# Kernel optimization log

Measured on AMD Instinct MI355X. Metric: run time of the kernel, lower is better.

Reference implementation:

```python
import jax, jax.numpy as jnp
import numpy as np

FEAT_STRIDE = 16
NMS_THRESH = 0.7
PRE_NMS = 6000   # eval mode: n_test_pre_nms
POST_NMS = 300   # eval mode: n_test_post_nms
MIN_SIZE = 16
NEG = jnp.float32(-1e30)


def _base_anchors(base_size=16, ratios=(0.5, 1.0, 2.0), scales=(8, 16, 32)):
    ctr = (base_size - 1) / 2.0
    size = float(base_size * base_size)
    out = []
    for r in ratios:
        w = np.round(np.sqrt(size / r))
        h = np.round(w * r)
        for s in scales:
            ws, hs = w * s, h * s
            out.append([ctr - 0.5 * (ws - 1), ctr - 0.5 * (hs - 1),
                        ctr + 0.5 * (ws - 1), ctr + 0.5 * (hs - 1)])
    return np.asarray(out, dtype=np.float32)  # (9,4)


def _all_anchors(feat_h, feat_w):
    base = _base_anchors()
    sx = np.arange(feat_w, dtype=np.float32) * FEAT_STRIDE
    sy = np.arange(feat_h, dtype=np.float32) * FEAT_STRIDE
    gx, gy = np.meshgrid(sx, sy)                      # (H,W)
    shifts = np.stack([gx, gy, gx, gy], axis=-1).reshape(-1, 1, 4)
    anchors = (shifts + base[None, :, :]).reshape(-1, 4)  # (H*W*9,4), order (h,w,a)
    return jnp.asarray(anchors)


def _nms_keep(boxes):
    # boxes sorted by descending score; torchvision IoU convention (no +1)
    n = boxes.shape[0]
    area = (boxes[:, 2] - boxes[:, 0]) * (boxes[:, 3] - boxes[:, 1])
    lt = jnp.maximum(boxes[:, None, :2], boxes[None, :, :2])  # (N,N,2)
    rb = jnp.minimum(boxes[:, None, 2:], boxes[None, :, 2:])
    wh = jnp.clip(rb - lt, 0.0)
    inter = wh[..., 0] * wh[..., 1]
    iou = inter / (area[:, None] + area[None, :] - inter)
    over = iou > NMS_THRESH
    idx = jnp.arange(n)

    def body(i, supp):
        row = over[i] & (idx > i) & jnp.logical_not(supp[i])
        return supp | row

    supp = jax.lax.fori_loop(0, n, body, jnp.zeros((n,), bool))
    keep = jnp.nonzero(~supp, size=POST_NMS, fill_value=0)[0]
    return keep


def reference(rpn_cls_scores, rpn_bbox_preds, img_h, img_w):
    feat_h, feat_w = rpn_cls_scores.shape[2], rpn_cls_scores.shape[3]
    anchors = _all_anchors(feat_h, feat_w)                      # (K,4)
    scores = jax.nn.softmax(
        rpn_cls_scores.transpose(0, 2, 3, 1).reshape(-1, 2), axis=1)[:, 1]
    deltas = rpn_bbox_preds.transpose(0, 2, 3, 1).reshape(-1, 4)

    widths = anchors[:, 2] - anchors[:, 0] + 1.0
    heights = anchors[:, 3] - anchors[:, 1] + 1.0
    ctr_x = anchors[:, 0] + 0.5 * widths
    ctr_y = anchors[:, 1] + 0.5 * heights
    dx, dy, dw, dh = deltas[:, 0], deltas[:, 1], deltas[:, 2], deltas[:, 3]
    pcx = dx * widths + ctr_x
    pcy = dy * heights + ctr_y
    pw = jnp.exp(dw) * widths
    ph = jnp.exp(dh) * heights

    x1 = jnp.clip(pcx - 0.5 * pw, 0.0, img_w - 1)
    y1 = jnp.clip(pcy - 0.5 * ph, 0.0, img_h - 1)
    x2 = jnp.clip(pcx + 0.5 * pw, 0.0, img_w - 1)
    y2 = jnp.clip(pcy + 0.5 * ph, 0.0, img_h - 1)
    proposals = jnp.stack([x1, y1, x2, y2], axis=1)             # (K,4)

    valid = ((x2 - x1 + 1.0) >= MIN_SIZE) & ((y2 - y1 + 1.0) >= MIN_SIZE)
    masked = jnp.where(valid, scores, NEG)
    _, order = jax.lax.top_k(masked, PRE_NMS)                   # sort desc + pre-nms cut
    boxes = proposals[order]                                    # (PRE_NMS,4)

    keep = _nms_keep(boxes)
    kept = boxes[keep]                                          # (POST_NMS,4)
    batch_inds = jnp.zeros((POST_NMS, 1), dtype=kept.dtype)
    return jnp.concatenate([batch_inds, kept], axis=1)          # (POST_NMS,5)


def setup_inputs() -> dict:
    key = jax.random.key(0)
    k1, k2 = jax.random.split(key)
    rpn_cls_scores = jax.random.normal(k1, (1, 18, 64, 100), dtype=jnp.float32)
    rpn_bbox_preds = 0.2 * jax.random.normal(k2, (1, 36, 64, 100), dtype=jnp.float32)
    return {"rpn_cls_scores": rpn_cls_scores, "rpn_bbox_preds": rpn_bbox_preds,
            "img_h": 1024, "img_w": 1600}
```

## Files before the change

### kernel.cpp

```cpp
#include <hip/hip_runtime.h>

typedef unsigned long long u64;
typedef unsigned int u32;

#define FEAT_W 100
#define NANCH 9
#define NTOT 57600
#define NPAD 65536
#define PRE_NMS 6000
#define POST_NMS 300
#define NBLK 94
#define NCHUNK 24
#define CH_STRIDE 6400
#define CHUNK 1024
#define CAP 6144

__constant__ double c_base[9][4] = {
    {-84.0, -40.0, 99.0, 55.0},    {-176.0, -88.0, 191.0, 103.0},
    {-360.0, -184.0, 375.0, 199.0},{-56.0, -56.0, 71.0, 71.0},
    {-120.0, -120.0, 135.0, 135.0},{-248.0, -248.0, 263.0, 263.0},
    {-36.0, -80.0, 51.0, 95.0},    {-80.0, -168.0, 95.0, 183.0},
    {-168.0, -344.0, 183.0, 359.0}};

struct BoxD { double x1, y1, x2, y2; };

__device__ __forceinline__ int packed_off(int i) {
  int q = i >> 6, r = i & 63;
  return 94 * i - 32 * q * (q - 1) - r * q;
}

__device__ __forceinline__ BoxD decode_box(int i, const float* __restrict__ bbox,
                                           double imw1, double imh1) {
  int pos = i / NANCH;
  int a = i - pos * NANCH;
  int h = pos / FEAT_W;
  int w = pos - h * FEAT_W;
  double ax1 = c_base[a][0] + 16.0 * (double)w;
  double ay1 = c_base[a][1] + 16.0 * (double)h;
  double ax2 = c_base[a][2] + 16.0 * (double)w;
  double ay2 = c_base[a][3] + 16.0 * (double)h;
  double wd = ax2 - ax1 + 1.0;
  double hg = ay2 - ay1 + 1.0;
  double cx = ax1 + 0.5 * wd;
  double cy = ay1 + 0.5 * hg;
  const float* bp = bbox + (size_t)(4 * a) * CH_STRIDE + pos;
  double dx = (double)bp[0];
  double dy = (double)bp[CH_STRIDE];
  double dw = (double)bp[2 * CH_STRIDE];
  double dh = (double)bp[3 * CH_STRIDE];
  double pcx = dx * wd + cx;
  double pcy = dy * hg + cy;
  double pw = exp(dw) * wd;
  double ph = exp(dh) * hg;
  BoxD b;
  b.x1 = fmin(fmax(pcx - 0.5 * pw, 0.0), imw1);
  b.y1 = fmin(fmax(pcy - 0.5 * ph, 0.0), imh1);
  b.x2 = fmin(fmax(pcx + 0.5 * pw, 0.0), imw1);
  b.y2 = fmin(fmax(pcy + 0.5 * ph, 0.0), imh1);
  return b;
}

__device__ __forceinline__ u64 score_key(int i, const float* __restrict__ cls,
                                         const float* __restrict__ bbox,
                                         double imw1, double imh1) {
  BoxD b = decode_box(i, bbox, imw1, imh1);
  bool valid = (b.x2 - b.x1 + 1.0 >= 16.0) && (b.y2 - b.y1 + 1.0 >= 16.0);
  int pos = i / NANCH;
  int a = i - pos * NANCH;
  double c0 = (double)cls[(size_t)(2 * a) * CH_STRIDE + pos];
  double c1 = (double)cls[(size_t)(2 * a + 1) * CH_STRIDE + pos];
  double m = fmax(c0, c1);
  double e0 = exp(c0 - m), e1 = exp(c1 - m);
  double s = e1 / (e0 + e1);
  double masked = valid ? s : (double)(-1e30f);
  u64 u = (u64)__double_as_longlong(masked);
  return (u >> 63) ? ~u : (u | 0x8000000000000000ULL);
}

__device__ __forceinline__ bool before(u64 ka, u32 va, u64 kb, u32 vb) {
  return (ka > kb) || (ka == kb && va < vb);
}
__device__ __forceinline__ bool comes_after(u64 ka, u32 va, u64 kb, u32 vb) {
  return (ka < kb) || (ka == kb && va > vb);
}

__global__ __launch_bounds__(512) void k_score_sort(
    const float* __restrict__ cls, const float* __restrict__ bbox,
    const int* __restrict__ imh, const int* __restrict__ imw,
    u64* __restrict__ keys, u32* __restrict__ vals) {
  __shared__ u64 sk[CHUNK];
  __shared__ u32 sv[CHUNK];
  int base = blockIdx.x * CHUNK;
  double imh1 = (double)(imh[0] - 1);
  double imw1 = (double)(imw[0] - 1);
  for (int t = threadIdx.x; t < CHUNK; t += 512) {
    int i = base + t;
    if (i < NTOT) { sk[t] = score_key(i, cls, bbox, imw1, imh1); sv[t] = (u32)i; }
    else { sk[t] = 0ULL; sv[t] = (u32)i; }
  }
  __syncthreads();
  bool prev_cross = false;
  for (int k = 2; k <= CHUNK; k <<= 1) {
    for (int j = k >> 1; j > 0; j >>= 1) {
      bool cross = (j >= 128);
      if (cross || prev_cross) __syncthreads();
      int t = threadIdx.x;
      int i = ((t & ~(j - 1)) << 1) | (t & (j - 1));
      int l = i | j;
      bool up = ((i & k) == 0);
      u64 ka = sk[i], kb = sk[l];
      u32 va = sv[i], vb = sv[l];
      if (comes_after(ka, va, kb, vb) == up) { sk[i] = kb; sv[i] = vb; sk[l] = ka; sv[l] = va; }
      prev_cross = cross;
    }
  }
  __syncthreads();
  for (int t = threadIdx.x; t < CHUNK; t += 512) { keys[base + t] = sk[t]; vals[base + t] = sv[t]; }
}


__global__ void k_merge1(const u64* __restrict__ Ak, const u32* __restrict__ Av,
                         u64* __restrict__ Bk, u32* __restrict__ Bv) {
  int gtid = blockIdx.x * blockDim.x + threadIdx.x;
  if (gtid >= NPAD) return;
  int lst = gtid >> 10, pos = gtid & 1023, grp = lst >> 2;
  u64 k = Ak[gtid]; u32 v = Av[gtid];
  int b0 = grp << 2;
  int q = lst & 3;
  int i0 = 0 + (0 >= q), i1 = 1 + (1 >= q), i2 = 2 + (2 >= q);
  const u64* K0 = Ak + (size_t)(b0 + i0) * 1024;
  const u64* K1 = Ak + (size_t)(b0 + i1) * 1024;
  const u64* K2 = Ak + (size_t)(b0 + i2) * 1024;
  const u32* V0 = Av + (size_t)(b0 + i0) * 1024;
  const u32* V1 = Av + (size_t)(b0 + i1) * 1024;
  const u32* V2 = Av + (size_t)(b0 + i2) * 1024;
  int lo0 = 0, hi0 = 1024, lo1 = 0, hi1 = 1024, lo2 = 0, hi2 = 1024;
  #pragma unroll
  for (int st = 0; st < 11; ++st) {
    int m0 = (lo0 + hi0) >> 1, m1 = (lo1 + hi1) >> 1, m2 = (lo2 + hi2) >> 1;
    int c0 = min(m0, 1023), c1 = min(m1, 1023), c2 = min(m2, 1023);
    u64 k0 = K0[c0], k1 = K1[c1], k2 = K2[c2];
    u32 v0 = V0[c0], v1 = V1[c1], v2 = V2[c2];
    if (lo0 < hi0) { if (before(k0, v0, k, v)) lo0 = m0 + 1; else hi0 = m0; }
    if (lo1 < hi1) { if (before(k1, v1, k, v)) lo1 = m1 + 1; else hi1 = m1; }
    if (lo2 < hi2) { if (before(k2, v2, k, v)) lo2 = m2 + 1; else hi2 = m2; }
  }
  int rank = pos + lo0 + lo1 + lo2;
  Bk[(size_t)grp * 4096 + rank] = k;
  Bv[(size_t)grp * 4096 + rank] = v;
}

__global__ void k_merge2(const u64* __restrict__ Bk, const u32* __restrict__ Bv,
                         u64* __restrict__ Ak, u32* __restrict__ Av) {
  int gtid = blockIdx.x * blockDim.x + threadIdx.x;
  if (gtid >= NPAD) return;
  int lst = gtid >> 12, pos = gtid & 4095, grp = lst >> 2;
  u64 k = Bk[gtid]; u32 v = Bv[gtid];
  int b0 = grp << 2;
  int q = lst & 3;
  int i0 = 0 + (0 >= q), i1 = 1 + (1 >= q), i2 = 2 + (2 >= q);
  const u64* K0 = Bk + (size_t)(b0 + i0) * 4096;
  const u64* K1 = Bk + (size_t)(b0 + i1) * 4096;
  const u64* K2 = Bk + (size_t)(b0 + i2) * 4096;
  const u32* V0 = Bv + (size_t)(b0 + i0) * 4096;
  const u32* V1 = Bv + (size_t)(b0 + i1) * 4096;
  const u32* V2 = Bv + (size_t)(b0 + i2) * 4096;
  int lo0 = 0, hi0 = 4096, lo1 = 0, hi1 = 4096, lo2 = 0, hi2 = 4096;
  #pragma unroll
  for (int st = 0; st < 13; ++st) {
    int m0 = (lo0 + hi0) >> 1, m1 = (lo1 + hi1) >> 1, m2 = (lo2 + hi2) >> 1;
    int c0 = min(m0, 4095), c1 = min(m1, 4095), c2 = min(m2, 4095);
    u64 k0 = K0[c0], k1 = K1[c1], k2 = K2[c2];
    u32 v0 = V0[c0], v1 = V1[c1], v2 = V2[c2];
    if (lo0 < hi0) { if (before(k0, v0, k, v)) lo0 = m0 + 1; else hi0 = m0; }
    if (lo1 < hi1) { if (before(k1, v1, k, v)) lo1 = m1 + 1; else hi1 = m1; }
    if (lo2 < hi2) { if (before(k2, v2, k, v)) lo2 = m2 + 1; else hi2 = m2; }
  }
  int rank = pos + lo0 + lo1 + lo2;
  if (rank < CAP) { Ak[(size_t)grp * CAP + rank] = k; Av[(size_t)grp * CAP + rank] = v; }
}

__global__ void k_merge3(const u64* __restrict__ Ak, const u32* __restrict__ Av,
                         const float* __restrict__ bbox, const int* __restrict__ imh,
                         const int* __restrict__ imw, double4* __restrict__ sboxes) {
  int gtid = blockIdx.x * blockDim.x + threadIdx.x;
  if (gtid >= 4 * CAP) return;
  int lst = gtid / CAP, pos = gtid - lst * CAP;
  u64 k = Ak[gtid]; u32 v = Av[gtid];
  int i0 = 0 + (0 >= lst), i1 = 1 + (1 >= lst), i2 = 2 + (2 >= lst);
  const u64* K0 = Ak + (size_t)i0 * CAP;
  const u64* K1 = Ak + (size_t)i1 * CAP;
  const u64* K2 = Ak + (size_t)i2 * CAP;
  const u32* V0 = Av + (size_t)i0 * CAP;
  const u32* V1 = Av + (size_t)i1 * CAP;
  const u32* V2 = Av + (size_t)i2 * CAP;
  int lo0 = 0, hi0 = CAP, lo1 = 0, hi1 = CAP, lo2 = 0, hi2 = CAP;
  #pragma unroll
  for (int st = 0; st < 13; ++st) {
    int m0 = (lo0 + hi0) >> 1, m1 = (lo1 + hi1) >> 1, m2 = (lo2 + hi2) >> 1;
    int c0 = min(m0, CAP - 1), c1 = min(m1, CAP - 1), c2 = min(m2, CAP - 1);
    u64 k0 = K0[c0], k1 = K1[c1], k2 = K2[c2];
    u32 v0 = V0[c0], v1 = V1[c1], v2 = V2[c2];
    if (lo0 < hi0) { if (before(k0, v0, k, v)) lo0 = m0 + 1; else hi0 = m0; }
    if (lo1 < hi1) { if (before(k1, v1, k, v)) lo1 = m1 + 1; else hi1 = m1; }
    if (lo2 < hi2) { if (before(k2, v2, k, v)) lo2 = m2 + 1; else hi2 = m2; }
  }
  int rank = pos + lo0 + lo1 + lo2;
  if (rank < PRE_NMS) {
    double imh1 = (double)(imh[0] - 1);
    double imw1 = (double)(imw[0] - 1);
    BoxD b = decode_box((int)v, bbox, imw1, imh1);
    sboxes[rank] = make_double4(b.x1, b.y1, b.x2, b.y2);
  }
}

__global__ void k_mask(const double4* __restrict__ sboxes, u64* __restrict__ mask,
                       u64* __restrict__ colC) {
  __shared__ double4 cb[64];
  int bc = blockIdx.x, br = blockIdx.y;
  int t = threadIdx.x;
  bool samechunk = (bc >> 2) == (br >> 2);
  if (bc < br) {
    if (samechunk) colC[(size_t)(((bc << 6) + t) * 4 + (br & 3))] = 0;
    return;
  }
  int j0 = bc * 64;
  int jt = j0 + t;
  cb[t] = (jt < PRE_NMS) ? sboxes[jt] : make_double4(0.0, 0.0, 0.0, 0.0);
  __syncthreads();
  int i = br * 64 + t;
  u64 bits = 0;
  if (i < PRE_NMS) {
    double4 rb = sboxes[i];
    double areai = (rb.z - rb.x) * (rb.w - rb.y);
    int cmax = min(64, PRE_NMS - j0);
    for (int c = 0; c < cmax; ++c) {
      int j = j0 + c;
      if (j <= i) continue;
      double4 cbx = cb[c];
      double xx1 = fmax(rb.x, cbx.x), yy1 = fmax(rb.y, cbx.y);
      double xx2 = fmin(rb.z, cbx.z), yy2 = fmin(rb.w, cbx.w);
      double w = fmax(xx2 - xx1, 0.0), h = fmax(yy2 - yy1, 0.0);
      double inter = w * h;
      double areaj = (cbx.z - cbx.x) * (cbx.w - cbx.y);
      if (inter > 0.7 * (areai + areaj - inter)) bits |= (1ULL << c);
    }
    mask[(size_t)(packed_off(i) + (bc - br))] = bits;
  }
  if (samechunk) {
    u64 colbits = 0;
    for (int j2 = 0; j2 < 64; ++j2) {
      u64 bl = __ballot(((bits >> j2) & 1ULL) != 0);
      if (t == j2) colbits = bl;
    }
    colC[(size_t)(((bc << 6) + t) * 4 + (br & 3))] = colbits;
  }
}

__device__ __forceinline__ u64 valid_word(int w) {
  int base = w << 6;
  if (base >= PRE_NMS) return 0ULL;
  if (base + 64 <= PRE_NMS) return ~0ULL;
  return (1ULL << (PRE_NMS - base)) - 1ULL;
}

__global__ __launch_bounds__(64) void k_scan(const u64* __restrict__ mask,
                                             const u64* __restrict__ colC,
                                             const double4* __restrict__ sboxes,
                                             float* __restrict__ out) {
  __shared__ int keepIdx[384];
  __shared__ int keepA[384];
  int lane = threadIdx.x;
  for (int r = lane; r < 384; r += 64) { keepIdx[r] = 0; keepA[r] = 0; }
  int nkeep = 0;
  bool done = false;

  u64 ct00, ct01, ct02, ct03, ct10, ct11, ct12, ct13;
  u64 ct20, ct21, ct22, ct23, ct30, ct31, ct32, ct33;

#define COL_LOAD(cc, T, a0, a1, a2, a3)                                        \
  {                                                                            \
    int J_ = ((cc) << 8) + ((T) << 6) + lane;                                  \
    a0 = 0; a1 = 0; a2 = 0; a3 = 0;                                            \
    if (J_ < PRE_NMS) {                                                        \
      const ulonglong2* p_ = (const ulonglong2*)(colC + (size_t)J_ * 4);       \
      ulonglong2 x_ = p_[0], y_ = p_[1];                                       \
      a0 = x_.x; a1 = x_.y; a2 = y_.x; a3 = y_.y;                              \
    }                                                                          \
  }

  COL_LOAD(0, 0, ct00, ct01, ct02, ct03)
  COL_LOAD(0, 1, ct10, ct11, ct12, ct13)
  COL_LOAD(0, 2, ct20, ct21, ct22, ct23)
  COL_LOAD(0, 3, ct30, ct31, ct32, ct33)

  for (int c = 0; c < NCHUNK && !done; ++c) {
    int wbase = c << 2;
    bool tail_ok = (wbase + 2) < NBLK;

    u64 n00 = 0, n01 = 0, n02 = 0, n03 = 0, n10 = 0, n11 = 0, n12 = 0, n13 = 0;
    u64 n20 = 0, n21 = 0, n22 = 0, n23 = 0, n30 = 0, n31 = 0, n32 = 0, n33 = 0;
    if (c + 1 < NCHUNK) {
      COL_LOAD(c + 1, 0, n00, n01, n02, n03)
      COL_LOAD(c + 1, 1, n10, n11, n12, n13)
      COL_LOAD(c + 1, 2, n20, n21, n22, n23)
      COL_LOAD(c + 1, 3, n30, n31, n32, n33)
    }

    int nq = (nkeep + 63) >> 6;
    int a0 = keepA[lane], a1 = keepA[64 + lane], a2 = keepA[128 + lane];
    int a3 = keepA[192 + lane], a4 = keepA[256 + lane];
    u64 g00 = 0, g01 = 0, g02 = 0, g03 = 0;
    u64 g10 = 0, g11 = 0, g12 = 0, g13 = 0;
    u64 g20 = 0, g21 = 0, g22 = 0, g23 = 0;
    u64 g30 = 0, g31 = 0, g32 = 0, g33 = 0;
    u64 g40 = 0, g41 = 0, g42 = 0, g43 = 0;
#define GATHER(AA, x0, x1, x2, x3)                                             \
    {                                                                          \
      const u64* p_ = mask + (size_t)(AA) + wbase;                             \
      x0 = p_[0];                                                              \
      x1 = p_[1];                                                              \
      if (tail_ok) { x2 = p_[2]; x3 = p_[3]; }                                 \
    }
    if (nq > 0) GATHER(a0, g00, g01, g02, g03)
    if (nq > 1) GATHER(a1, g10, g11, g12, g13)
    if (nq > 2) GATHER(a2, g20, g21, g22, g23)
    if (nq > 3) GATHER(a3, g30, g31, g32, g33)
    if (nq > 4) GATHER(a4, g40, g41, g42, g43)
#undef GATHER
    u64 or0 = 0, or1 = 0, or2 = 0, or3 = 0;
    if (lane < nkeep)       { or0 |= g00; or1 |= g01; or2 |= g02; or3 |= g03; }
    if (64 + lane < nkeep)  { or0 |= g10; or1 |= g11; or2 |= g12; or3 |= g13; }
    if (128 + lane < nkeep) { or0 |= g20; or1 |= g21; or2 |= g22; or3 |= g23; }
    if (192 + lane < nkeep) { or0 |= g30; or1 |= g31; or2 |= g32; or3 |= g33; }
    if (256 + lane < nkeep) { or0 |= g40; or1 |= g41; or2 |= g42; or3 |= g43; }
    #pragma unroll
    for (int m = 32; m; m >>= 1) {
      or0 |= __shfl_xor(or0, m);
      or1 |= __shfl_xor(or1, m);
      or2 |= __shfl_xor(or2, m);
      or3 |= __shfl_xor(or3, m);
    }

    u64 kf0 = 0, kf1 = 0, kf2 = 0, kf3 = 0;

#define RUN_WORD(OR_, TT, DIAGC, CROSS_EXPR, KFVAR)                            \
    if (!done) {                                                               \
      u64 alive = ~(OR_) & valid_word(wbase + (TT));                           \
      alive &= ~__ballot((CROSS_EXPR) != 0ULL);                                \
      u64 kfacc = 0;                                                           \
      while (alive) {                                                          \
        int b = __builtin_ctzll(alive);                                        \
        u64 bb = 1ULL << b;                                                    \
        kfacc |= bb;                                                           \
        u64 sup_ = __ballot((((DIAGC) >> b) & 1ULL) != 0ULL);                  \
        alive &= ~(sup_ | bb);                                                 \
      }                                                                        \
      KFVAR = kfacc;                                                           \
      if (kfacc) {                                                             \
        if ((kfacc >> lane) & 1ULL) {                                          \
          int idx = nkeep + __popcll(kfacc & ((1ULL << lane) - 1ULL));         \
          if (idx < 384) {                                                     \
            int K = (c << 8) + ((TT) << 6) + lane;                             \
            keepIdx[idx] = K;                                                  \
            keepA[idx] = packed_off(K) - (K >> 6);                             \
          }                                                                    \
        }                                                                      \
        nkeep += __popcll(kfacc);                                              \
        if (nkeep >= POST_NMS) done = true;                                    \
      }                                                                        \
    }

    RUN_WORD(or0, 0, ct00, 0ULL, kf0)
    RUN_WORD(or1, 1, ct11, (ct10 & kf0), kf1)
    RUN_WORD(or2, 2, ct22, (ct20 & kf0) | (ct21 & kf1), kf2)
    RUN_WORD(or3, 3, ct33, (ct30 & kf0) | (ct31 & kf1) | (ct32 & kf2), kf3)
#undef RUN_WORD
    (void)kf3;

    ct00 = n00; ct01 = n01; ct02 = n02; ct03 = n03;
    ct10 = n10; ct11 = n11; ct12 = n12; ct13 = n13;
    ct20 = n20; ct21 = n21; ct22 = n22; ct23 = n23;
    ct30 = n30; ct31 = n31; ct32 = n32; ct33 = n33;
  }
#undef COL_LOAD
  __syncthreads();

  for (int r = lane; r < POST_NMS; r += 64) {
    int kk = keepIdx[r];
    double4 b = sboxes[kk];
    float* o = out + r * 5;
    o[0] = 0.0f;
    o[1] = (float)b.x;
    o[2] = (float)b.y;
    o[3] = (float)b.z;
    o[4] = (float)b.w;
  }
}

extern "C" void kernel_launch(void* const* d_in, const int* in_sizes, int n_in,
                              void* d_out, int out_size, void* d_ws, size_t ws_size,
                              hipStream_t stream) {
  const float* cls = (const float*)d_in[0];
  const float* bbox = (const float*)d_in[1];
  const int* imh = (const int*)d_in[2];
  const int* imw = (const int*)d_in[3];
  float* out = (float*)d_out;

  char* p = (char*)d_ws;
  double4* sboxes = (double4*)p;
  u64* colC = (u64*)(p + 192512);
  char* mb = p + 385024;
  u64* maskbuf = (u64*)mb;
  u64* Ak = (u64*)mb;
  u32* Av = (u32*)(mb + 524288);
  u64* Bk = (u64*)(mb + 786432);
  u32* Bv = (u32*)(mb + 1310720);

  k_score_sort<<<64, 512, 0, stream>>>(cls, bbox, imh, imw, Ak, Av);
  k_merge1<<<NPAD / 256, 256, 0, stream>>>(Ak, Av, Bk, Bv);
  k_merge2<<<NPAD / 256, 256, 0, stream>>>(Bk, Bv, Ak, Av);
  k_merge3<<<(4 * CAP) / 256, 256, 0, stream>>>(Ak, Av, bbox, imh, imw, sboxes);
  k_mask<<<dim3(NBLK, NBLK), 64, 0, stream>>>(sboxes, maskbuf, colC);
  k_scan<<<1, 64, 0, stream>>>(maskbuf, colC, sboxes, out);
}
```

Baseline: 145.0 us.

## Use float32 boxes for IoU and prefetch next-chunk suppression gathers in NMS scan

Boxes are now stored and compared as float32 instead of double, with IoU computed by division to match the reference convention. This halves box memory traffic and avoids slow FP64 math in the mask kernel. The serial scan now gathers the next chunk's suppression words incrementally: earlier keeps are gathered before the current chunk's serial resolution and only new keeps afterward, so gather latency overlaps the serial work. Float precision may flip borderline IoU comparisons relative to the previous double path.

```diff
diff --git a/kernel.cpp b/kernel.cpp
--- a/kernel.cpp
+++ b/kernel.cpp
@@ -118,7 +118,6 @@
   for (int t = threadIdx.x; t < CHUNK; t += 512) { keys[base + t] = sk[t]; vals[base + t] = sv[t]; }
 }
 
-
 __global__ void k_merge1(const u64* __restrict__ Ak, const u32* __restrict__ Av,
                          u64* __restrict__ Bk, u32* __restrict__ Bv) {
   int gtid = blockIdx.x * blockDim.x + threadIdx.x;
@@ -182,7 +181,7 @@
 
 __global__ void k_merge3(const u64* __restrict__ Ak, const u32* __restrict__ Av,
                          const float* __restrict__ bbox, const int* __restrict__ imh,
-                         const int* __restrict__ imw, double4* __restrict__ sboxes) {
+                         const int* __restrict__ imw, float4* __restrict__ fboxes) {
   int gtid = blockIdx.x * blockDim.x + threadIdx.x;
   if (gtid >= 4 * CAP) return;
   int lst = gtid / CAP, pos = gtid - lst * CAP;
@@ -210,13 +209,13 @@
     double imh1 = (double)(imh[0] - 1);
     double imw1 = (double)(imw[0] - 1);
     BoxD b = decode_box((int)v, bbox, imw1, imh1);
-    sboxes[rank] = make_double4(b.x1, b.y1, b.x2, b.y2);
-  }
-}
-
-__global__ void k_mask(const double4* __restrict__ sboxes, u64* __restrict__ mask,
+    fboxes[rank] = make_float4((float)b.x1, (float)b.y1, (float)b.x2, (float)b.y2);
+  }
+}
+
+__global__ void k_mask(const float4* __restrict__ fboxes, u64* __restrict__ mask,
                        u64* __restrict__ colC) {
-  __shared__ double4 cb[64];
+  __shared__ float4 cb[64];
   int bc = blockIdx.x, br = blockIdx.y;
   int t = threadIdx.x;
   bool samechunk = (bc >> 2) == (br >> 2);
@@ -226,24 +225,25 @@
   }
   int j0 = bc * 64;
   int jt = j0 + t;
-  cb[t] = (jt < PRE_NMS) ? sboxes[jt] : make_double4(0.0, 0.0, 0.0, 0.0);
+  cb[t] = (jt < PRE_NMS) ? fboxes[jt] : make_float4(0.f, 0.f, 0.f, 0.f);
   __syncthreads();
   int i = br * 64 + t;
   u64 bits = 0;
   if (i < PRE_NMS) {
-    double4 rb = sboxes[i];
-    double areai = (rb.z - rb.x) * (rb.w - rb.y);
+    float4 rb = fboxes[i];
+    float areai = (rb.z - rb.x) * (rb.w - rb.y);
     int cmax = min(64, PRE_NMS - j0);
     for (int c = 0; c < cmax; ++c) {
       int j = j0 + c;
       if (j <= i) continue;
-      double4 cbx = cb[c];
-      double xx1 = fmax(rb.x, cbx.x), yy1 = fmax(rb.y, cbx.y);
-      double xx2 = fmin(rb.z, cbx.z), yy2 = fmin(rb.w, cbx.w);
-      double w = fmax(xx2 - xx1, 0.0), h = fmax(yy2 - yy1, 0.0);
-      double inter = w * h;
-      double areaj = (cbx.z - cbx.x) * (cbx.w - cbx.y);
-      if (inter > 0.7 * (areai + areaj - inter)) bits |= (1ULL << c);
+      float4 cbx = cb[c];
+      float xx1 = fmaxf(rb.x, cbx.x), yy1 = fmaxf(rb.y, cbx.y);
+      float xx2 = fminf(rb.z, cbx.z), yy2 = fminf(rb.w, cbx.w);
+      float w = fmaxf(xx2 - xx1, 0.0f), h = fmaxf(yy2 - yy1, 0.0f);
+      float inter = w * h;
+      float areaj = (cbx.z - cbx.x) * (cbx.w - cbx.y);
+      float iou = inter / (areai + areaj - inter);
+      if (iou > 0.7f) bits |= (1ULL << c);
     }
     mask[(size_t)(packed_off(i) + (bc - br))] = bits;
   }
@@ -266,7 +266,7 @@
 
 __global__ __launch_bounds__(64) void k_scan(const u64* __restrict__ mask,
                                              const u64* __restrict__ colC,
-                                             const double4* __restrict__ sboxes,
+                                             const float4* __restrict__ fboxes,
                                              float* __restrict__ out) {
   __shared__ int keepIdx[384];
   __shared__ int keepA[384];
@@ -274,18 +274,20 @@
   for (int r = lane; r < 384; r += 64) { keepIdx[r] = 0; keepA[r] = 0; }
   int nkeep = 0;
   bool done = false;
+  int a0 = 0, a1 = 0, a2 = 0, a3 = 0, a4 = 0;
+  u64 or0 = 0, or1 = 0, or2 = 0, or3 = 0;
 
   u64 ct00, ct01, ct02, ct03, ct10, ct11, ct12, ct13;
   u64 ct20, ct21, ct22, ct23, ct30, ct31, ct32, ct33;
 
-#define COL_LOAD(cc, T, a0, a1, a2, a3)                                        \
+#define COL_LOAD(cc, T, x0, x1, x2, x3)                                        \
   {                                                                            \
     int J_ = ((cc) << 8) + ((T) << 6) + lane;                                  \
-    a0 = 0; a1 = 0; a2 = 0; a3 = 0;                                            \
+    x0 = 0; x1 = 0; x2 = 0; x3 = 0;                                            \
     if (J_ < PRE_NMS) {                                                        \
       const ulonglong2* p_ = (const ulonglong2*)(colC + (size_t)J_ * 4);       \
-      ulonglong2 x_ = p_[0], y_ = p_[1];                                       \
-      a0 = x_.x; a1 = x_.y; a2 = y_.x; a3 = y_.y;                              \
+      ulonglong2 u_ = p_[0], w_ = p_[1];                                       \
+      x0 = u_.x; x1 = u_.y; x2 = w_.x; x3 = w_.y;                              \
     }                                                                          \
   }
 
@@ -296,50 +298,34 @@
 
   for (int c = 0; c < NCHUNK && !done; ++c) {
     int wbase = c << 2;
-    bool tail_ok = (wbase + 2) < NBLK;
+    int wnext = wbase + 4;
+    bool gnext = (c + 1 < NCHUNK);
+    bool tail_n = (wnext + 2) < NBLK;
+    int oldn = nkeep;
 
     u64 n00 = 0, n01 = 0, n02 = 0, n03 = 0, n10 = 0, n11 = 0, n12 = 0, n13 = 0;
     u64 n20 = 0, n21 = 0, n22 = 0, n23 = 0, n30 = 0, n31 = 0, n32 = 0, n33 = 0;
-    if (c + 1 < NCHUNK) {
+    if (gnext) {
       COL_LOAD(c + 1, 0, n00, n01, n02, n03)
       COL_LOAD(c + 1, 1, n10, n11, n12, n13)
       COL_LOAD(c + 1, 2, n20, n21, n22, n23)
       COL_LOAD(c + 1, 3, n30, n31, n32, n33)
     }
 
-    int nq = (nkeep + 63) >> 6;
-    int a0 = keepA[lane], a1 = keepA[64 + lane], a2 = keepA[128 + lane];
-    int a3 = keepA[192 + lane], a4 = keepA[256 + lane];
-    u64 g00 = 0, g01 = 0, g02 = 0, g03 = 0;
-    u64 g10 = 0, g11 = 0, g12 = 0, g13 = 0;
-    u64 g20 = 0, g21 = 0, g22 = 0, g23 = 0;
-    u64 g30 = 0, g31 = 0, g32 = 0, g33 = 0;
-    u64 g40 = 0, g41 = 0, g42 = 0, g43 = 0;
-#define GATHER(AA, x0, x1, x2, x3)                                             \
-    {                                                                          \
-      const u64* p_ = mask + (size_t)(AA) + wbase;                             \
-      x0 = p_[0];                                                              \
-      x1 = p_[1];                                                              \
-      if (tail_ok) { x2 = p_[2]; x3 = p_[3]; }                                 \
-    }
-    if (nq > 0) GATHER(a0, g00, g01, g02, g03)
-    if (nq > 1) GATHER(a1, g10, g11, g12, g13)
-    if (nq > 2) GATHER(a2, g20, g21, g22, g23)
-    if (nq > 3) GATHER(a3, g30, g31, g32, g33)
-    if (nq > 4) GATHER(a4, g40, g41, g42, g43)
-#undef GATHER
-    u64 or0 = 0, or1 = 0, or2 = 0, or3 = 0;
-    if (lane < nkeep)       { or0 |= g00; or1 |= g01; or2 |= g02; or3 |= g03; }
-    if (64 + lane < nkeep)  { or0 |= g10; or1 |= g11; or2 |= g12; or3 |= g13; }
-    if (128 + lane < nkeep) { or0 |= g20; or1 |= g21; or2 |= g22; or3 |= g23; }
-    if (192 + lane < nkeep) { or0 |= g30; or1 |= g31; or2 |= g32; or3 |= g33; }
-    if (256 + lane < nkeep) { or0 |= g40; or1 |= g41; or2 |= g42; or3 |= g43; }
-    #pragma unroll
-    for (int m = 32; m; m >>= 1) {
-      or0 |= __shfl_xor(or0, m);
-      or1 |= __shfl_xor(or1, m);
-      or2 |= __shfl_xor(or2, m);
-      or3 |= __shfl_xor(or3, m);
+    u64 e0 = 0, e1 = 0, e2 = 0, e3 = 0;
+    if (gnext) {
+#define EGATHER(AA, LIM)                                                       \
+      if ((LIM) < oldn) {                                                      \
+        const u64* p_ = mask + (size_t)(AA) + wnext;                           \
+        e0 |= p_[0]; e1 |= p_[1];                                              \
+        if (tail_n) { e2 |= p_[2]; e3 |= p_[3]; }                              \
+      }
+      EGATHER(a0, lane)
+      EGATHER(a1, 64 + lane)
+      EGATHER(a2, 128 + lane)
+      EGATHER(a3, 192 + lane)
+      EGATHER(a4, 256 + lane)
+#undef EGATHER
     }
 
     u64 kf0 = 0, kf1 = 0, kf2 = 0, kf3 = 0;
@@ -378,6 +364,34 @@
 #undef RUN_WORD
     (void)kf3;
 
+    if (gnext && !done) {
+      int nk = min(nkeep, 384);
+#define LGATHER(AR, SLOT)                                                      \
+      {                                                                        \
+        int s_ = (SLOT);                                                       \
+        if (s_ >= oldn && s_ < nk) {                                           \
+          AR = keepA[s_];                                                      \
+          const u64* p_ = mask + (size_t)AR + wnext;                           \
+          e0 |= p_[0]; e1 |= p_[1];                                            \
+          if (tail_n) { e2 |= p_[2]; e3 |= p_[3]; }                            \
+        }                                                                      \
+      }
+      LGATHER(a0, lane)
+      LGATHER(a1, 64 + lane)
+      LGATHER(a2, 128 + lane)
+      LGATHER(a3, 192 + lane)
+      LGATHER(a4, 256 + lane)
+#undef LGATHER
+      #pragma unroll
+      for (int m = 32; m; m >>= 1) {
+        e0 |= __shfl_xor(e0, m);
+        e1 |= __shfl_xor(e1, m);
+        e2 |= __shfl_xor(e2, m);
+        e3 |= __shfl_xor(e3, m);
+      }
+      or0 = e0; or1 = e1; or2 = e2; or3 = e3;
+    }
+
     ct00 = n00; ct01 = n01; ct02 = n02; ct03 = n03;
     ct10 = n10; ct11 = n11; ct12 = n12; ct13 = n13;
     ct20 = n20; ct21 = n21; ct22 = n22; ct23 = n23;
@@ -388,13 +402,13 @@
 
   for (int r = lane; r < POST_NMS; r += 64) {
     int kk = keepIdx[r];
-    double4 b = sboxes[kk];
+    float4 b = fboxes[kk];
     float* o = out + r * 5;
     o[0] = 0.0f;
-    o[1] = (float)b.x;
-    o[2] = (float)b.y;
-    o[3] = (float)b.z;
-    o[4] = (float)b.w;
+    o[1] = b.x;
+    o[2] = b.y;
+    o[3] = b.z;
+    o[4] = b.w;
   }
 }
 
@@ -408,8 +422,8 @@
   float* out = (float*)d_out;
 
   char* p = (char*)d_ws;
-  double4* sboxes = (double4*)p;
-  u64* colC = (u64*)(p + 192512);
+  float4* fboxes = (float4*)p;
+  u64* colC = (u64*)(p + 96256);
   char* mb = p + 385024;
   u64* maskbuf = (u64*)mb;
   u64* Ak = (u64*)mb;
@@ -420,7 +434,7 @@
   k_score_sort<<<64, 512, 0, stream>>>(cls, bbox, imh, imw, Ak, Av);
   k_merge1<<<NPAD / 256, 256, 0, stream>>>(Ak, Av, Bk, Bv);
   k_merge2<<<NPAD / 256, 256, 0, stream>>>(Bk, Bv, Ak, Av);
-  k_merge3<<<(4 * CAP) / 256, 256, 0, stream>>>(Ak, Av, bbox, imh, imw, sboxes);
-  k_mask<<<dim3(NBLK, NBLK), 64, 0, stream>>>(sboxes, maskbuf, colC);
-  k_scan<<<1, 64, 0, stream>>>(maskbuf, colC, sboxes, out);
-}
+  k_merge3<<<(4 * CAP) / 256, 256, 0, stream>>>(Ak, Av, bbox, imh, imw, fboxes);
+  k_mask<<<dim3(NBLK, NBLK), 64, 0, stream>>>(fboxes, maskbuf, colC);
+  k_scan<<<1, 64, 0, stream>>>(maskbuf, colC, fboxes, out);
+}
```

New measurement: 148.5 us. +2.4%, slower.
